# Optimization experiments

Hardware: AMD Instinct MI355X
Metric: run time of the kernel (lower is better)

Reference implementation:

```python
import jax, jax.numpy as jnp
import numpy as np

B, HH, WW, E = 8, 64, 64, 384
NH, EXP = 6, 2
D1 = (EXP * E) // NH * NH      # 768
HD = D1 // NH                  # 128
RPE = 512
LAYERS = 3
EPS = 1e-6


def srms(x):
    # SimpleRMSNorm: no learnable weight
    return x * jax.lax.rsqrt(jnp.mean(x * x, axis=-1, keepdims=True) + EPS)


def rpe_forward(pos, pw, pb, lw, lb, ow, ob):
    # pos: (n, 1) -> (n, NH*HD). Rpe MLP: act(pos_proj) -> layers x [norm,act,linear] -> out
    x = jax.nn.relu(pos @ pw + pb)
    for i in range(lw.shape[0]):  # fixed small layer count
        x = jax.nn.relu(srms(x)) @ lw[i] + lb[i]
    return jax.nn.relu(srms(x)) @ ow + ob


def tno_coeffs(n, pw, pb, lw, lb, ow, ob):
    # Toeplitz coeffs t_0..t_{n-1}, t_0(dummy), t_{-(n-1)}..t_{-1} for circular conv of len 2n
    pos = jnp.arange(1, n, dtype=jnp.float32)[:, None]             # (n-1, 1), par_type=1
    neg = -jnp.arange(1, n, dtype=jnp.float32)[::-1][:, None]      # -(n-1)..-1
    zero = jnp.zeros((1, 1), dtype=jnp.float32)
    t_zero = rpe_forward(zero, pw, pb, lw, lb, ow, ob)             # (1, NH*HD)
    t_pos = rpe_forward(pos, pw, pb, lw, lb, ow, ob)               # (n-1, NH*HD)
    t_neg = rpe_forward(neg, pw, pb, lw, lb, ow, ob)
    a = jnp.concatenate([t_zero, t_pos, t_zero, t_neg], axis=0)    # (2n, NH*HD)
    return a.reshape(2 * n, NH, HD).transpose(1, 0, 2)             # (NH, 2n, HD)


def tno_apply(v, a, axis):
    # v: (b, h, H, W, d); FFT-based Toeplitz (circular) mixing along `axis` in {-3, -2}
    n = v.shape[axis]
    a = a[:, :, None, :] if axis == -3 else a[:, None, :, :]
    y = jnp.fft.rfft(v, 2 * n, axis=axis)
    af = jnp.fft.rfft(a, 2 * n, axis=axis)
    out = jnp.fft.irfft(af * y, 2 * n, axis=axis)
    return jax.lax.slice_in_dim(out, 0, n, axis=out.ndim + axis)


def setup_inputs() -> dict:
    key = jax.random.key(0)
    ks = jax.random.split(key, 24)
    s = 0.02
    def rn(k, shape):
        return jax.random.normal(k, shape, dtype=jnp.float32) * s
    inp = {
        "x": jax.random.normal(ks[0], (B, HH, WW, E), dtype=jnp.float32),
        "H": HH, "W": WW,
        "Wu": rn(ks[1], (E, D1)), "bu": jnp.zeros((D1,), jnp.float32),
        "Wv": rn(ks[2], (E, D1)), "bv": jnp.zeros((D1,), jnp.float32),
        "Wo": rn(ks[3], (D1, E)), "bo": jnp.zeros((E,), jnp.float32),
    }
    for t, off in (("r1", 4), ("r2", 10)):
        inp[t + "_pw"] = rn(ks[off], (1, RPE))
        inp[t + "_pb"] = jnp.zeros((RPE,), jnp.float32)
        inp[t + "_lw"] = rn(ks[off + 1], (LAYERS, RPE, RPE))
        inp[t + "_lb"] = jnp.zeros((LAYERS, RPE), jnp.float32)
        inp[t + "_ow"] = rn(ks[off + 2], (RPE, NH * HD))
        inp[t + "_ob"] = jnp.zeros((NH * HD,), jnp.float32)
    return inp


def reference(x, H, W, Wu, bu, Wv, bv, Wo, bo,
              r1_pw, r1_pb, r1_lw, r1_lb, r1_ow, r1_ob,
              r2_pw, r2_pb, r2_lw, r2_lb, r2_ow, r2_ob):
    b = x.shape[0]
    xn = srms(x)                                    # pre_norm (SimpleRMSNorm)
    u = jax.nn.silu(xn @ Wu + bu)                   # gate branch
    v = jax.nn.silu(xn @ Wv + bv)
    v = v.reshape(b, H, W, NH, HD).transpose(0, 3, 1, 2, 4)        # b h H W d
    a_h = tno_coeffs(H, r2_pw, r2_pb, r2_lw, r2_lb, r2_ow, r2_ob)  # toep2, dim=-3
    a_w = tno_coeffs(W, r1_pw, r1_pb, r1_lw, r1_lb, r1_ow, r1_ob)  # toep1, dim=-2
    out = tno_apply(v, a_h, -3) + tno_apply(v, a_w, -2)
    out = out.transpose(0, 2, 3, 1, 4).reshape(b, H, W, NH * HD)   # b H W (h d)
    out = u * out
    return out @ Wo + bo + x
```

## Files before the change

kernel.cpp:

```cpp
#include <hip/hip_runtime.h>
#include <stdint.h>


typedef __attribute__((ext_vector_type(4))) float  f32x4;
typedef __attribute__((ext_vector_type(8))) short  s16x8;
typedef __attribute__((ext_vector_type(8))) unsigned short u16x8;
typedef __attribute__((ext_vector_type(4))) unsigned short u16x4;
typedef unsigned short u16;

#define M_TOT 32768

__device__ __forceinline__ u16 f2bf(float f) {
  union { float f; unsigned int u; } v; v.f = f;
  unsigned int r = (v.u + 0x7FFFu + ((v.u >> 16) & 1u)) >> 16;
  return (u16)r;
}
__device__ __forceinline__ float bf2f(u16 h) {
  union { unsigned int u; float f; } v; v.u = ((unsigned int)h) << 16;
  return v.f;
}
__device__ __forceinline__ float silu_f(float x) {
  return x * __builtin_amdgcn_rcpf(1.f + __expf(-x));
}

__device__ __forceinline__ void gload_lds16(const u16* g, u16* l) {
  __builtin_amdgcn_global_load_lds(
      (const __attribute__((address_space(1))) uint32_t*)g,
      (__attribute__((address_space(3))) uint32_t*)l, 16, 0, 0);
}

__global__ __launch_bounds__(256) void setup_k(
    const float* __restrict__ x, u16* __restrict__ xn,
    const float* __restrict__ Wu, const float* __restrict__ Wv,
    const float* __restrict__ Wo, u16* __restrict__ Wuvt, u16* __restrict__ Wot,
    const float* __restrict__ r1lw, const float* __restrict__ r1ow,
    const float* __restrict__ r2lw, const float* __restrict__ r2ow,
    u16* __restrict__ lwT, u16* __restrict__ owT,
    const float* __restrict__ r1pw, const float* __restrict__ r1pb,
    const float* __restrict__ r2pw, const float* __restrict__ r2pb,
    float* __restrict__ X0) {
  __shared__ float sm[32][33];
  const int bid = blockIdx.x;
  const int tid = threadIdx.x;

  if (bid < 8192) {
    int row  = bid * 4 + (tid >> 6);
    int lane = tid & 63;
    const float* xr = x + (size_t)row * 384 + lane;
    float v[6]; float ss = 0.f;
#pragma unroll
    for (int i = 0; i < 6; i++) { v[i] = xr[i * 64]; ss += v[i] * v[i]; }
#pragma unroll
    for (int off = 32; off > 0; off >>= 1) ss += __shfl_xor(ss, off);
    float sc = rsqrtf(ss * (1.f / 384.f) + 1e-6f);
    u16* o = xn + (size_t)row * 384 + lane;
#pragma unroll
    for (int i = 0; i < 6; i++) o[i * 64] = f2bf(v[i] * sc);
  } else if (bid < 11360) {
    int b = bid - 8192;
    const float* src; u16* dst; int C, DS, R0, C0;
    if (b < 2304) {
      int mlp = b / 1152, r = b % 1152;
      if (r < 768) {
        int L = r / 256, t = r % 256;
        R0 = (t / 16) * 32; C0 = (t % 16) * 32;
        src = (mlp ? r2lw : r1lw) + (size_t)L * 262144;
        dst = lwT + (size_t)(mlp * 3 + L) * 262144;
        C = 512; DS = 512;
      } else {
        int t = r - 768;
        R0 = (t / 24) * 32; C0 = (t % 24) * 32;
        src = mlp ? r2ow : r1ow;
        dst = owT + (size_t)mlp * 393216;
        C = 768; DS = 512;
      }
    } else {
      int t = b - 2304;
      if (t < 288)      { R0 = (t / 24) * 32; C0 = (t % 24) * 32;
                          src = Wu; C = 768; dst = Wuvt;             DS = 384; }
      else if (t < 576) { int t2 = t - 288; R0 = (t2 / 24) * 32; C0 = (t2 % 24) * 32;
                          src = Wv; C = 768; dst = Wuvt + 768 * 384; DS = 384; }
      else              { int t2 = t - 576; R0 = (t2 / 12) * 32; C0 = (t2 % 12) * 32;
                          src = Wo; C = 384; dst = Wot;              DS = 768; }
    }
    int lx = tid % 32, ly = tid / 32;
#pragma unroll
    for (int q = 0; q < 4; q++) {
      int y = q * 8 + ly;
      sm[y][lx] = src[(size_t)(R0 + y) * C + C0 + lx];
    }
    __syncthreads();
#pragma unroll
    for (int q = 0; q < 4; q++) {
      int y = q * 8 + ly;
      dst[(size_t)(C0 + y) * DS + R0 + lx] = f2bf(sm[lx][y]);
    }
  } else {
    int idx = (bid - 11360) * 256 + tid;
    int gid = idx * 4;
    int row = gid >> 9, col = gid & 511;
    int mlp = row >> 7, p = row & 127;
    float pos = (p < 64) ? (float)p : ((p == 64) ? 0.f : (float)(p - 128));
    const float* pw = (mlp ? r2pw : r1pw) + col;
    const float* pb = (mlp ? r2pb : r1pb) + col;
    f32x4 w = *(const f32x4*)pw;
    f32x4 bb = *(const f32x4*)pb;
    f32x4 o;
#pragma unroll
    for (int e = 0; e < 4; e++) o[e] = fmaxf(pos * w[e] + bb[e], 0.f);
    *(f32x4*)(X0 + gid) = o;
  }
}

template <int N, bool TOUT>
__global__ __launch_bounds__(256) void rpe_layer_k(
    const float* __restrict__ X,
    const u16* __restrict__ wtA, const u16* __restrict__ wtB,
    const float* __restrict__ bA, const float* __restrict__ bB,
    float* __restrict__ outA, float* __restrict__ outB) {
  constexpr int NSL = N / 64;
  const int mlp = blockIdx.x / NSL;
  const int n0  = (blockIdx.x % NSL) * 64;
  const u16* WT = mlp ? wtB : wtA;
  const float* bias = mlp ? bB : bA;
  float* out = mlp ? outB : outA;
  const float* Xm = X + (size_t)mlp * 128 * 512;

  __shared__ __align__(16) u16 Bs[64 * 512];
  __shared__ __align__(16) u16 As[2][128 * 64];
  __shared__ float scale[128];

  const int tid  = threadIdx.x;
  const int lane = tid & 63;
  const int w    = tid >> 6;
  const int fl   = lane & 15, fh = lane >> 4;

#pragma unroll
  for (int r = 0; r < 16; r++) {
    int row  = r * 4 + w;
    int csrc = (lane & ~7) | ((lane & 7) ^ (row & 7));
    gload_lds16(WT + (size_t)(n0 + row) * 512 + csrc * 8,
                Bs + row * 512 + lane * 8);
  }

  {
    int row = tid >> 1, half = tid & 1;
    const float* xr = Xm + (size_t)row * 512 + half * 256;
    float ss = 0.f;
#pragma unroll 8
    for (int q = 0; q < 64; q++) {
      f32x4 v = *(const f32x4*)(xr + q * 4);
      ss += v[0] * v[0] + v[1] * v[1] + v[2] * v[2] + v[3] * v[3];
    }
    ss += __shfl_xor(ss, 1);
    if (!half) scale[row] = rsqrtf(ss * (1.f / 512.f) + 1e-6f);
  }
  __syncthreads();

  int arow[4], akc[4];
  float s_[4];
#pragma unroll
  for (int q = 0; q < 4; q++) {
    int cid = q * 256 + tid;
    arow[q] = cid >> 3;
    akc[q]  = cid & 7;
    s_[q]   = scale[arow[q]];
  }

#pragma unroll
  for (int q = 0; q < 4; q++) {
    const float* xp = Xm + (size_t)arow[q] * 512 + akc[q] * 8;
    f32x4 v0 = *(const f32x4*)xp;
    f32x4 v1 = *(const f32x4*)(xp + 4);
    u16x8 pk;
#pragma unroll
    for (int e = 0; e < 4; e++) pk[e]     = f2bf(fmaxf(v0[e], 0.f) * s_[q]);
#pragma unroll
    for (int e = 0; e < 4; e++) pk[4 + e] = f2bf(fmaxf(v1[e], 0.f) * s_[q]);
    *(u16x8*)(&As[0][arow[q] * 64 + ((akc[q] ^ (arow[q] & 7)) * 8)]) = pk;
  }
  __syncthreads();

  f32x4 acc[2][4];
  {
    f32x4 z = {0.f, 0.f, 0.f, 0.f};
#pragma unroll
    for (int i = 0; i < 2; i++)
#pragma unroll
      for (int j = 0; j < 4; j++) acc[i][j] = z;
  }

  for (int kti = 0; kti < 8; kti++) {
    const int cur = kti & 1;
    f32x4 pf0[4], pf1[4];
    if (kti < 7) {
#pragma unroll
      for (int q = 0; q < 4; q++) {
        const float* xp = Xm + (size_t)arow[q] * 512 + (kti + 1) * 64 + akc[q] * 8;
        pf0[q] = *(const f32x4*)xp;
        pf1[q] = *(const f32x4*)(xp + 4);
      }
    }
#pragma unroll
    for (int ks = 0; ks < 2; ks++) {
      const int xc = ((ks * 4 + fh) ^ (fl & 7)) * 8;
      s16x8 af[2], bfr[4];
#pragma unroll
      for (int i = 0; i < 2; i++)
        af[i] = *(const s16x8*)(&As[cur][(w * 32 + i * 16 + fl) * 64 + xc]);
#pragma unroll
      for (int j = 0; j < 4; j++)
        bfr[j] = *(const s16x8*)(&Bs[(j * 16 + fl) * 512 + kti * 64 + xc]);
#pragma unroll
      for (int i = 0; i < 2; i++)
#pragma unroll
        for (int j = 0; j < 4; j++)
          acc[i][j] = __builtin_amdgcn_mfma_f32_16x16x32_bf16(af[i], bfr[j], acc[i][j], 0, 0, 0);
    }
    if (kti < 7) {
#pragma unroll
      for (int q = 0; q < 4; q++) {
        u16x8 pk;
#pragma unroll
        for (int e = 0; e < 4; e++) pk[e]     = f2bf(fmaxf(pf0[q][e], 0.f) * s_[q]);
#pragma unroll
        for (int e = 0; e < 4; e++) pk[4 + e] = f2bf(fmaxf(pf1[q][e], 0.f) * s_[q]);
        *(u16x8*)(&As[cur ^ 1][arow[q] * 64 + ((akc[q] ^ (arow[q] & 7)) * 8)]) = pk;
      }
    }
    __syncthreads();
  }

#pragma unroll
  for (int i = 0; i < 2; i++)
#pragma unroll
    for (int j = 0; j < 4; j++) {
      int c = n0 + j * 16 + fl;
      float bv_ = bias[c];
#pragma unroll
      for (int q = 0; q < 4; q++) {
        int r = w * 32 + i * 16 + fh * 4 + q;
        if (TOUT) out[(size_t)c * 128 + r] = acc[i][j][q] + bv_;
        else      out[(size_t)r * N + c]   = acc[i][j][q] + bv_;
      }
    }
}

__global__ __launch_bounds__(256) void gemm0_k(
    const u16* __restrict__ A, const u16* __restrict__ Bt,
    u16* __restrict__ u_out, u16* __restrict__ vt_out,
    const float* __restrict__ bu, const float* __restrict__ bv) {
  __shared__ __align__(16) char smem[34816];
  u16*   As  = (u16*)smem;
  u16*   Bs  = As + 128 * 64;
  float* epi = (float*)smem;

  const int tid  = threadIdx.x;
  const int lane = tid & 63;
  const int wid  = tid >> 6;
  const int wm   = wid >> 1, wn = wid & 1;
  const int bm   = blockIdx.x & 255, bn = blockIdx.x >> 8;
  const int m0   = bm * 128, n0 = bn * 128;
  const int fl   = lane & 15, fh = lane >> 4;
  const int K    = 384;

  f32x4 acc[4][4];
  {
    f32x4 z = {0.f, 0.f, 0.f, 0.f};
#pragma unroll
    for (int i = 0; i < 4; i++)
#pragma unroll
      for (int j = 0; j < 4; j++) acc[i][j] = z;
  }

  const int sr  = tid >> 3;
  const int scl = (tid & 7) * 8;
  const int scs = ((tid & 7) ^ (sr & 7)) * 8;

  for (int kt = 0; kt < K; kt += 64) {
    const u16* gA = A  + (size_t)(m0 + sr) * K + kt + scs;
    const u16* gB = Bt + (size_t)(n0 + sr) * K + kt + scs;
    u16* lA = As + sr * 64 + scl;
    u16* lB = Bs + sr * 64 + scl;
#pragma unroll
    for (int i = 0; i < 4; i++) {
      gload_lds16(gA + (size_t)(i * 32) * K, lA + i * 32 * 64);
      gload_lds16(gB + (size_t)(i * 32) * K, lB + i * 32 * 64);
    }
    __syncthreads();
#pragma unroll
    for (int ks = 0; ks < 2; ks++) {
      s16x8 af[4], bfr[4];
      const int xc = ((ks * 4 + fh) ^ (fl & 7)) * 8;
      const u16* ap = As + (wm * 64 + fl) * 64 + xc;
      const u16* bp = Bs + (wn * 64 + fl) * 64 + xc;
#pragma unroll
      for (int i = 0; i < 4; i++) af[i] = *(const s16x8*)(ap + i * 16 * 64);
#pragma unroll
      for (int j = 0; j < 4; j++) bfr[j] = *(const s16x8*)(bp + j * 16 * 64);
#pragma unroll
      for (int i = 0; i < 4; i++)
#pragma unroll
        for (int j = 0; j < 4; j++)
          acc[i][j] = __builtin_amdgcn_mfma_f32_16x16x32_bf16(af[i], bfr[j], acc[i][j], 0, 0, 0);
    }
    __syncthreads();
  }

  for (int half = 0; half < 2; half++) {
    __syncthreads();
    if (wm == half) {
#pragma unroll
      for (int i = 0; i < 4; i++)
#pragma unroll
        for (int j = 0; j < 4; j++) {
          int er = i * 16 + fh * 4;
          int ec = wn * 64 + j * 16 + fl;
#pragma unroll
          for (int q = 0; q < 4; q++) epi[(er + q) * 132 + ec] = acc[i][j][q];
        }
    }
    __syncthreads();
    const bool isU = (n0 < 768);
    u16* baseo = isU ? u_out : vt_out;
    const int cc = tid >> 1;
    const int cg = (isU ? n0 : n0 - 768) + cc;
    const float bias_v = (isU ? bu : bv)[cg];
    u16* dst = baseo + (size_t)cg * M_TOT + m0 + half * 64;
#pragma unroll
    for (int q = 0; q < 4; q++) {
      int mb = (tid & 1) * 8 + q * 16;
      u16x8 pk;
#pragma unroll
      for (int e = 0; e < 8; e++) {
        int mm = mb + e;
        pk[e] = f2bf(silu_f(epi[mm * 132 + cc] + bias_v));
      }
      *(u16x8*)(dst + mb) = pk;
    }
  }
}

__global__ __launch_bounds__(512, 2) void gemm2_k(
    const u16* __restrict__ gT, const u16* __restrict__ Wot,
    float* __restrict__ out, const float* __restrict__ bo,
    const float* __restrict__ xres) {
  __shared__ __align__(16) u16 As[128 * 64];
  __shared__ __align__(16) u16 Bs[384 * 64];

  const int tid  = threadIdx.x;
  const int lane = tid & 63;
  const int wid  = tid >> 6;
  const int wm   = wid >> 2;
  const int wn   = wid & 3;
  const int m0   = blockIdx.x * 128;
  const int fl   = lane & 15, fh = lane >> 4;

  f32x4 acc[4][6];
  {
    f32x4 z = {0.f, 0.f, 0.f, 0.f};
#pragma unroll
    for (int i = 0; i < 4; i++)
#pragma unroll
      for (int j = 0; j < 6; j++) acc[i][j] = z;
  }

  const int sr  = tid >> 3;
  const int scl = (tid & 7) * 8;
  const int scs = ((tid & 7) ^ (sr & 7)) * 8;

  for (int kt = 0; kt < 768; kt += 64) {
#pragma unroll
    for (int i = 0; i < 6; i++)
      gload_lds16(Wot + (size_t)(sr + 64 * i) * 768 + kt + scs,
                  Bs + (sr + 64 * i) * 64 + scl);
#pragma unroll
    for (int r = 0; r < 2; r++) {
      int cid = r * 512 + tid;
      int row = cid >> 4;
      int cm  = cid & 15;
      const u16* ga = gT + (size_t)(kt + row) * M_TOT + m0 + cm * 8;
      u16x8 rv = *(const u16x8*)ga;
      int kc = row >> 3, of = row & 7;
#pragma unroll
      for (int e = 0; e < 8; e++)
        As[(cm * 8 + e) * 64 + ((kc ^ e) << 3) + of] = rv[e];
    }
    __syncthreads();
#pragma unroll
    for (int ks = 0; ks < 2; ks++) {
      s16x8 af[4], bfr[6];
      const int xc = ((ks * 4 + fh) ^ (fl & 7)) * 8;
      const u16* ap = As + (wm * 64 + fl) * 64 + xc;
      const u16* bp = Bs + (wn * 96 + fl) * 64 + xc;
#pragma unroll
      for (int i = 0; i < 4; i++) af[i] = *(const s16x8*)(ap + i * 16 * 64);
#pragma unroll
      for (int j = 0; j < 6; j++) bfr[j] = *(const s16x8*)(bp + j * 16 * 64);
#pragma unroll
      for (int i = 0; i < 4; i++)
#pragma unroll
        for (int j = 0; j < 6; j++)
          acc[i][j] = __builtin_amdgcn_mfma_f32_16x16x32_bf16(af[i], bfr[j], acc[i][j], 0, 0, 0);
    }
    __syncthreads();
  }

  float bov[6];
#pragma unroll
  for (int j = 0; j < 6; j++) bov[j] = bo[wn * 96 + j * 16 + fl];
#pragma unroll
  for (int i = 0; i < 4; i++) {
#pragma unroll
    for (int q = 0; q < 4; q++) {
      int m = m0 + wm * 64 + i * 16 + fh * 4 + q;
      const float* xr = xres + (size_t)m * 384;
      float* orow = out + (size_t)m * 384;
#pragma unroll
      for (int j = 0; j < 6; j++) {
        int n = wn * 96 + j * 16 + fl;
        orow[n] = acc[i][j][q] + bov[j] + xr[n];
      }
    }
  }
}

__global__ __launch_bounds__(256) void conv_k(const u16* __restrict__ vt,
                                              const u16* __restrict__ ut,
                                              const float* __restrict__ a_hT,
                                              const float* __restrict__ a_wT,
                                              u16* __restrict__ gT) {
  __shared__ __align__(16) u16 Th[64 * 72];
  __shared__ __align__(16) u16 Tw[64 * 72];
  __shared__ __align__(16) u16 Vs[64 * 72];
  __shared__ __align__(16) u16 VTs[64 * 72];
  __shared__ __align__(16) u16 Us[64 * 72];
  __shared__ float ahr[192];
  __shared__ float awr[192];
  u16* epi = VTs;

  const int tid = threadIdx.x;
  const int c = blockIdx.x;
  const int lane = tid & 63, w = tid >> 6;
  const int fl = lane & 15, fh = lane >> 4;

  if (tid < 192) {
    int idx = (128 - tid) & 127;
    ahr[tid] = a_hT[(size_t)c * 128 + idx];
    awr[tid] = a_wT[(size_t)c * 128 + idx];
  }
  __syncthreads();

  {
    int y = tid & 63, j0 = (tid >> 6) * 16;
    int base = 128 - y + j0;
    u16x8 p0, p1, q0, q1;
#pragma unroll
    for (int e = 0; e < 8; e++) {
      p0[e] = f2bf(ahr[base + e]);
      p1[e] = f2bf(ahr[base + 8 + e]);
      q0[e] = f2bf(awr[base + e]);
      q1[e] = f2bf(awr[base + 8 + e]);
    }
    *(u16x8*)(Th + y * 72 + j0)     = p0;
    *(u16x8*)(Th + y * 72 + j0 + 8) = p1;
    *(u16x8*)(Tw + y * 72 + j0)     = q0;
    *(u16x8*)(Tw + y * 72 + j0 + 8) = q1;
  }

  const int sy = tid >> 2, sx = (tid & 3) * 16;
  const int ty = tid & 63, tj = (tid >> 6) * 16;

  for (int b = 0; b < 8; b++) {
    const u16* srcv = vt + (size_t)c * M_TOT + b * 4096;
    const u16* srcu = ut + (size_t)c * M_TOT + b * 4096;
    *(u16x8*)(Vs + sy * 72 + sx)     = *(const u16x8*)(srcv + sy * 64 + sx);
    *(u16x8*)(Vs + sy * 72 + sx + 8) = *(const u16x8*)(srcv + sy * 64 + sx + 8);
    *(u16x8*)(Us + sy * 72 + sx)     = *(const u16x8*)(srcu + sy * 64 + sx);
    *(u16x8*)(Us + sy * 72 + sx + 8) = *(const u16x8*)(srcu + sy * 64 + sx + 8);
    __syncthreads();

    {
      u16x8 q0 = *(const u16x8*)(Vs + ty * 72 + tj);
      u16x8 q1 = *(const u16x8*)(Vs + ty * 72 + tj + 8);
#pragma unroll
      for (int e = 0; e < 8; e++) VTs[(tj + e) * 72 + ty]     = q0[e];
#pragma unroll
      for (int e = 0; e < 8; e++) VTs[(tj + 8 + e) * 72 + ty] = q1[e];
    }
    __syncthreads();

    f32x4 acc[4];
    {
      f32x4 z = {0.f, 0.f, 0.f, 0.f};
#pragma unroll
      for (int i = 0; i < 4; i++) acc[i] = z;
    }
#pragma unroll
    for (int ks = 0; ks < 2; ks++) {
      s16x8 qh = *(const s16x8*)(Th + (w * 16 + fl) * 72 + ks * 32 + fh * 8);
#pragma unroll
      for (int i = 0; i < 4; i++) {
        s16x8 p = *(const s16x8*)(VTs + (i * 16 + fl) * 72 + ks * 32 + fh * 8);
        acc[i] = __builtin_amdgcn_mfma_f32_16x16x32_bf16(p, qh, acc[i], 0, 0, 0);
      }
      s16x8 qw = *(const s16x8*)(Vs + (w * 16 + fl) * 72 + ks * 32 + fh * 8);
#pragma unroll
      for (int i = 0; i < 4; i++) {
        s16x8 p = *(const s16x8*)(Tw + (i * 16 + fl) * 72 + ks * 32 + fh * 8);
        acc[i] = __builtin_amdgcn_mfma_f32_16x16x32_bf16(p, qw, acc[i], 0, 0, 0);
      }
    }
    __syncthreads();

    {
      int y = w * 16 + fl;
#pragma unroll
      for (int i = 0; i < 4; i++) {
        u16x4 uq = *(const u16x4*)(Us + y * 72 + i * 16 + fh * 4);
        u16x4 pk;
#pragma unroll
        for (int e = 0; e < 4; e++) pk[e] = f2bf(acc[i][e] * bf2f(uq[e]));
        *(u16x4*)(epi + y * 72 + i * 16 + fh * 4) = pk;
      }
    }
    __syncthreads();

    {
      u16x8 a0 = *(const u16x8*)(epi + sy * 72 + sx);
      u16x8 a1 = *(const u16x8*)(epi + sy * 72 + sx + 8);
      u16* dst = gT + (size_t)c * M_TOT + b * 4096 + sy * 64 + sx;
      *(u16x8*)dst = a0;
      *(u16x8*)(dst + 8) = a1;
    }
    __syncthreads();
  }
}

extern "C" void kernel_launch(void* const* d_in, const int* in_sizes, int n_in,
                              void* d_out, int out_size, void* d_ws, size_t ws_size,
                              hipStream_t stream) {
  const float* x    = (const float*)d_in[0];
  const float* Wu   = (const float*)d_in[3];
  const float* bu   = (const float*)d_in[4];
  const float* Wv   = (const float*)d_in[5];
  const float* bv   = (const float*)d_in[6];
  const float* Wo   = (const float*)d_in[7];
  const float* bo   = (const float*)d_in[8];
  const float* r1pw = (const float*)d_in[9];
  const float* r1pb = (const float*)d_in[10];
  const float* r1lw = (const float*)d_in[11];
  const float* r1lb = (const float*)d_in[12];
  const float* r1ow = (const float*)d_in[13];
  const float* r1ob = (const float*)d_in[14];
  const float* r2pw = (const float*)d_in[15];
  const float* r2pb = (const float*)d_in[16];
  const float* r2lw = (const float*)d_in[17];
  const float* r2lb = (const float*)d_in[18];
  const float* r2ow = (const float*)d_in[19];
  const float* r2ob = (const float*)d_in[20];
  float* outp = (float*)d_out;

  char* ws = (char*)d_ws;
  size_t off = 0;
  auto carve = [&](size_t bytes) {
    char* p = ws + off;
    off += (bytes + 255) & ~(size_t)255;
    return p;
  };
  u16*   xn   = (u16*)carve((size_t)M_TOT * 384 * 2);
  u16*   uT   = (u16*)carve((size_t)768 * M_TOT * 2);
  u16*   vT   = (u16*)carve((size_t)768 * M_TOT * 2);
  u16*   gT   = (u16*)carve((size_t)768 * M_TOT * 2);
  u16*   Wuvt = (u16*)carve((size_t)1536 * 384 * 2);
  u16*   Wot  = (u16*)carve((size_t)384 * 768 * 2);
  float* awT  = (float*)carve((size_t)768 * 128 * 4);
  float* ahT  = (float*)carve((size_t)768 * 128 * 4);

  char* rb  = (char*)gT;
  u16*   lwT = (u16*)rb;
  u16*   owT = (u16*)(rb + 3145728);
  float* X0  = (float*)(rb + 3145728 + 1572864);
  float* X1  = X0 + 256 * 512;

  setup_k<<<11488, 256, 0, stream>>>(x, xn, Wu, Wv, Wo, Wuvt, Wot,
                                     r1lw, r1ow, r2lw, r2ow, lwT, owT,
                                     r1pw, r1pb, r2pw, r2pb, X0);

  rpe_layer_k<512, false><<<16, 256, 0, stream>>>(X0, lwT, lwT + 3 * 262144,
                                                  r1lb, r2lb, X1, X1 + 128 * 512);
  rpe_layer_k<512, false><<<16, 256, 0, stream>>>(X1, lwT + 262144, lwT + 4 * 262144,
                                                  r1lb + 512, r2lb + 512, X0, X0 + 128 * 512);
  rpe_layer_k<512, false><<<16, 256, 0, stream>>>(X0, lwT + 2 * 262144, lwT + 5 * 262144,
                                                  r1lb + 1024, r2lb + 1024, X1, X1 + 128 * 512);
  rpe_layer_k<768, true><<<24, 256, 0, stream>>>(X1, owT, owT + 393216,
                                                 r1ob, r2ob, awT, ahT);

  gemm0_k<<<256 * 12, 256, 0, stream>>>(xn, Wuvt, uT, vT, bu, bv);
  conv_k<<<768, 256, 0, stream>>>(vT, uT, ahT, awT, gT);
  gemm2_k<<<256, 512, 0, stream>>>(gT, Wot, outp, bo, x);
}
```

Baseline: 366.3 us.

## Fuse RPE layers into one kernel, widen gemm0 tiles, prefetch conv inputs

```diff
diff --git a/kernel.cpp b/kernel.cpp
--- a/kernel.cpp
+++ b/kernel.cpp
@@ -112,6 +112,110 @@
   }
 }
 
+__global__ __launch_bounds__(1024) void rpe_all_k(
+    float* __restrict__ X0, float* __restrict__ X1,
+    const u16* __restrict__ lwT,
+    const float* __restrict__ r1lb, const float* __restrict__ r2lb) {
+  __shared__ __align__(16) u16 Bs[512 * 64];
+  __shared__ __align__(16) u16 As[128 * 64];
+  __shared__ float scale[128];
+
+  const int tid  = threadIdx.x;
+  const int mlp  = blockIdx.x;
+  const int lane = tid & 63;
+  const int w    = tid >> 6;
+  const int wm   = w >> 2;
+  const int wn   = w & 3;
+  const int fl   = lane & 15, fh = lane >> 4;
+  const float* lb = mlp ? r2lb : r1lb;
+
+  const int arow = tid >> 3, ac = tid & 7;
+  const int sqrow = tid >> 3, sqseg = tid & 7;
+
+  for (int L = 0; L < 3; L++) {
+    float* Xin  = (L & 1) ? X1 : X0;
+    float* Xout = (L & 1) ? X0 : X1;
+    const float* Xm = Xin + (size_t)mlp * 128 * 512;
+    float* Xo = Xout + (size_t)mlp * 128 * 512;
+    const u16* WT = lwT + (size_t)(mlp * 3 + L) * 262144;
+    const float* bias = lb + L * 512;
+
+    {
+      const float* xr = Xm + (size_t)sqrow * 512 + sqseg * 64;
+      float ss = 0.f;
+#pragma unroll
+      for (int q = 0; q < 16; q++) {
+        f32x4 v = *(const f32x4*)(xr + q * 4);
+        ss += v[0] * v[0] + v[1] * v[1] + v[2] * v[2] + v[3] * v[3];
+      }
+      ss += __shfl_xor(ss, 1);
+      ss += __shfl_xor(ss, 2);
+      ss += __shfl_xor(ss, 4);
+      if ((tid & 7) == 0) scale[sqrow] = rsqrtf(ss * (1.f / 512.f) + 1e-6f);
+    }
+    __syncthreads();
+
+    f32x4 acc[2][8];
+    {
+      f32x4 z = {0.f, 0.f, 0.f, 0.f};
+#pragma unroll
+      for (int i = 0; i < 2; i++)
+#pragma unroll
+        for (int j = 0; j < 8; j++) acc[i][j] = z;
+    }
+    const float s_ = scale[arow];
+
+    for (int kt = 0; kt < 512; kt += 64) {
+      {
+        const float* xp = Xm + (size_t)arow * 512 + kt + ac * 8;
+        f32x4 v0 = *(const f32x4*)xp;
+        f32x4 v1 = *(const f32x4*)(xp + 4);
+        u16x8 pk;
+#pragma unroll
+        for (int e = 0; e < 4; e++) pk[e]     = f2bf(fmaxf(v0[e], 0.f) * s_);
+#pragma unroll
+        for (int e = 0; e < 4; e++) pk[4 + e] = f2bf(fmaxf(v1[e], 0.f) * s_);
+        *(u16x8*)(&As[arow * 64 + ((ac ^ (arow & 7)) * 8)]) = pk;
+      }
+#pragma unroll
+      for (int q = 0; q < 4; q++) {
+        int id = q * 1024 + tid;
+        int row = id >> 3, c = id & 7;
+        gload_lds16(WT + (size_t)row * 512 + kt + ((c ^ (row & 7)) * 8),
+                    Bs + id * 8);
+      }
+      __syncthreads();
+#pragma unroll
+      for (int ks = 0; ks < 2; ks++) {
+        const int xc = ((ks * 4 + fh) ^ (fl & 7)) * 8;
+        s16x8 af0 = *(const s16x8*)(&As[(wm * 32 + fl) * 64 + xc]);
+        s16x8 af1 = *(const s16x8*)(&As[(wm * 32 + 16 + fl) * 64 + xc]);
+#pragma unroll
+        for (int j = 0; j < 8; j++) {
+          s16x8 bfr = *(const s16x8*)(&Bs[(wn * 128 + j * 16 + fl) * 64 + xc]);
+          acc[0][j] = __builtin_amdgcn_mfma_f32_16x16x32_bf16(af0, bfr, acc[0][j], 0, 0, 0);
+          acc[1][j] = __builtin_amdgcn_mfma_f32_16x16x32_bf16(af1, bfr, acc[1][j], 0, 0, 0);
+        }
+      }
+      __syncthreads();
+    }
+
+#pragma unroll
+    for (int i = 0; i < 2; i++)
+#pragma unroll
+      for (int j = 0; j < 8; j++) {
+        int c = wn * 128 + j * 16 + fl;
+        float bv_ = bias[c];
+#pragma unroll
+        for (int q = 0; q < 4; q++) {
+          int r = wm * 32 + i * 16 + fh * 4 + q;
+          Xo[(size_t)r * 512 + c] = acc[i][j][q] + bv_;
+        }
+      }
+    __syncthreads();
+  }
+}
+
 template <int N, bool TOUT>
 __global__ __launch_bounds__(256) void rpe_layer_k(
     const float* __restrict__ X,
@@ -246,11 +350,11 @@
     }
 }
 
-__global__ __launch_bounds__(256) void gemm0_k(
+__global__ __launch_bounds__(512) void gemm0_k(
     const u16* __restrict__ A, const u16* __restrict__ Bt,
     u16* __restrict__ u_out, u16* __restrict__ vt_out,
     const float* __restrict__ bu, const float* __restrict__ bv) {
-  __shared__ __align__(16) char smem[34816];
+  __shared__ __align__(16) char smem[49152];
   u16*   As  = (u16*)smem;
   u16*   Bs  = As + 128 * 64;
   float* epi = (float*)smem;
@@ -258,9 +362,10 @@
   const int tid  = threadIdx.x;
   const int lane = tid & 63;
   const int wid  = tid >> 6;
-  const int wm   = wid >> 1, wn = wid & 1;
+  const int wm   = wid >> 2;
+  const int wn   = wid & 3;
   const int bm   = blockIdx.x & 255, bn = blockIdx.x >> 8;
-  const int m0   = bm * 128, n0 = bn * 128;
+  const int m0   = bm * 128, n0 = bn * 256;
   const int fl   = lane & 15, fh = lane >> 4;
   const int K    = 384;
 
@@ -273,20 +378,17 @@
       for (int j = 0; j < 4; j++) acc[i][j] = z;
   }
 
-  const int sr  = tid >> 3;
-  const int scl = (tid & 7) * 8;
-  const int scs = ((tid & 7) ^ (sr & 7)) * 8;
+  const int ra = tid >> 3;
+  const int ca = tid & 7;
+  const int swc = (ca ^ (ra & 7)) * 8;
 
   for (int kt = 0; kt < K; kt += 64) {
-    const u16* gA = A  + (size_t)(m0 + sr) * K + kt + scs;
-    const u16* gB = Bt + (size_t)(n0 + sr) * K + kt + scs;
-    u16* lA = As + sr * 64 + scl;
-    u16* lB = Bs + sr * 64 + scl;
-#pragma unroll
-    for (int i = 0; i < 4; i++) {
-      gload_lds16(gA + (size_t)(i * 32) * K, lA + i * 32 * 64);
-      gload_lds16(gB + (size_t)(i * 32) * K, lB + i * 32 * 64);
-    }
+    gload_lds16(A + (size_t)(m0 + ra) * K + kt + swc,        As + ra * 64 + ca * 8);
+    gload_lds16(A + (size_t)(m0 + 64 + ra) * K + kt + swc,   As + (64 + ra) * 64 + ca * 8);
+#pragma unroll
+    for (int q = 0; q < 4; q++)
+      gload_lds16(Bt + (size_t)(n0 + q * 64 + ra) * K + kt + swc,
+                  Bs + (q * 64 + ra) * 64 + ca * 8);
     __syncthreads();
 #pragma unroll
     for (int ks = 0; ks < 2; ks++) {
@@ -307,36 +409,39 @@
     __syncthreads();
   }
 
-  for (int half = 0; half < 2; half++) {
-    __syncthreads();
-    if (wm == half) {
-#pragma unroll
-      for (int i = 0; i < 4; i++)
-#pragma unroll
-        for (int j = 0; j < 4; j++) {
-          int er = i * 16 + fh * 4;
-          int ec = wn * 64 + j * 16 + fl;
-#pragma unroll
-          for (int q = 0; q < 4; q++) epi[(er + q) * 132 + ec] = acc[i][j][q];
-        }
-    }
-    __syncthreads();
-    const bool isU = (n0 < 768);
-    u16* baseo = isU ? u_out : vt_out;
-    const int cc = tid >> 1;
-    const int cg = (isU ? n0 : n0 - 768) + cc;
-    const float bias_v = (isU ? bu : bv)[cg];
-    u16* dst = baseo + (size_t)cg * M_TOT + m0 + half * 64;
-#pragma unroll
-    for (int q = 0; q < 4; q++) {
-      int mb = (tid & 1) * 8 + q * 16;
-      u16x8 pk;
+#pragma unroll
+  for (int mh = 0; mh < 2; mh++) {
+#pragma unroll
+    for (int nh = 0; nh < 2; nh++) {
+      __syncthreads();
+      if (wm == mh && (wn >> 1) == nh) {
+        int nq = wn & 1;
+#pragma unroll
+        for (int i = 0; i < 4; i++)
+#pragma unroll
+          for (int j = 0; j < 4; j++) {
+            int er = i * 16 + fh * 4;
+            int ec = nq * 64 + j * 16 + fl;
+#pragma unroll
+            for (int q = 0; q < 4; q++) epi[(er + q) * 133 + ec] = acc[i][j][q];
+          }
+      }
+      __syncthreads();
+      int cc = tid >> 2;
+      int cg = n0 + nh * 128 + cc;
+      const bool isU = (cg < 768);
+      const int cgm = isU ? cg : cg - 768;
+      const float bias_v = (isU ? bu : bv)[cgm];
+      u16* dst = (isU ? u_out : vt_out) + (size_t)cgm * M_TOT + m0 + mh * 64 + (tid & 3) * 16;
+      u16x8 pk0, pk1;
+      const int mb = (tid & 3) * 16;
 #pragma unroll
       for (int e = 0; e < 8; e++) {
-        int mm = mb + e;
-        pk[e] = f2bf(silu_f(epi[mm * 132 + cc] + bias_v));
-      }
-      *(u16x8*)(dst + mb) = pk;
+        pk0[e] = f2bf(silu_f(epi[(mb + e) * 133 + cc] + bias_v));
+        pk1[e] = f2bf(silu_f(epi[(mb + 8 + e) * 133 + cc] + bias_v));
+      }
+      *(u16x8*)dst = pk0;
+      *(u16x8*)(dst + 8) = pk1;
     }
   }
 }
@@ -471,14 +576,29 @@
   const int sy = tid >> 2, sx = (tid & 3) * 16;
   const int ty = tid & 63, tj = (tid >> 6) * 16;
 
+  const u16* srcv0 = vt + (size_t)c * M_TOT;
+  const u16* srcu0 = ut + (size_t)c * M_TOT;
+
+  u16x8 pv0 = *(const u16x8*)(srcv0 + sy * 64 + sx);
+  u16x8 pv1 = *(const u16x8*)(srcv0 + sy * 64 + sx + 8);
+  u16x8 pu0 = *(const u16x8*)(srcu0 + sy * 64 + sx);
+  u16x8 pu1 = *(const u16x8*)(srcu0 + sy * 64 + sx + 8);
+
   for (int b = 0; b < 8; b++) {
-    const u16* srcv = vt + (size_t)c * M_TOT + b * 4096;
-    const u16* srcu = ut + (size_t)c * M_TOT + b * 4096;
-    *(u16x8*)(Vs + sy * 72 + sx)     = *(const u16x8*)(srcv + sy * 64 + sx);
-    *(u16x8*)(Vs + sy * 72 + sx + 8) = *(const u16x8*)(srcv + sy * 64 + sx + 8);
-    *(u16x8*)(Us + sy * 72 + sx)     = *(const u16x8*)(srcu + sy * 64 + sx);
-    *(u16x8*)(Us + sy * 72 + sx + 8) = *(const u16x8*)(srcu + sy * 64 + sx + 8);
-    __syncthreads();
+    *(u16x8*)(Vs + sy * 72 + sx)     = pv0;
+    *(u16x8*)(Vs + sy * 72 + sx + 8) = pv1;
+    *(u16x8*)(Us + sy * 72 + sx)     = pu0;
+    *(u16x8*)(Us + sy * 72 + sx + 8) = pu1;
+    __syncthreads();
+
+    if (b < 7) {
+      const u16* nv = srcv0 + (b + 1) * 4096 + sy * 64 + sx;
+      const u16* nu = srcu0 + (b + 1) * 4096 + sy * 64 + sx;
+      pv0 = *(const u16x8*)nv;
+      pv1 = *(const u16x8*)(nv + 8);
+      pu0 = *(const u16x8*)nu;
+      pu1 = *(const u16x8*)(nu + 8);
+    }
 
     {
       u16x8 q0 = *(const u16x8*)(Vs + ty * 72 + tj);
@@ -587,16 +707,11 @@
                                      r1lw, r1ow, r2lw, r2ow, lwT, owT,
                                      r1pw, r1pb, r2pw, r2pb, X0);
 
-  rpe_layer_k<512, false><<<16, 256, 0, stream>>>(X0, lwT, lwT + 3 * 262144,
-                                                  r1lb, r2lb, X1, X1 + 128 * 512);
-  rpe_layer_k<512, false><<<16, 256, 0, stream>>>(X1, lwT + 262144, lwT + 4 * 262144,
-                                                  r1lb + 512, r2lb + 512, X0, X0 + 128 * 512);
-  rpe_layer_k<512, false><<<16, 256, 0, stream>>>(X0, lwT + 2 * 262144, lwT + 5 * 262144,
-                                                  r1lb + 1024, r2lb + 1024, X1, X1 + 128 * 512);
+  rpe_all_k<<<2, 1024, 0, stream>>>(X0, X1, lwT, r1lb, r2lb);
   rpe_layer_k<768, true><<<24, 256, 0, stream>>>(X1, owT, owT + 393216,
                                                  r1ob, r2ob, awT, ahT);
 
-  gemm0_k<<<256 * 12, 256, 0, stream>>>(xn, Wuvt, uT, vT, bu, bv);
+  gemm0_k<<<256 * 6, 512, 0, stream>>>(xn, Wuvt, uT, vT, bu, bv);
   conv_k<<<768, 256, 0, stream>>>(vT, uT, ahT, awT, gT);
   gemm2_k<<<256, 512, 0, stream>>>(gT, Wot, outp, bo, x);
 }
```

New measurement: 478.5 us. 30.6% more time.
